# Kernel optimization log

Hardware: AMD Instinct MI355X
Metric: run time of the kernel (lower is better)

## Reference

```python
import jax, jax.numpy as jnp
import numpy as np


def setup_inputs() -> dict:
    key = jax.random.key(0)
    kq, kk, kv = jax.random.split(key, 3)
    shape = (4, 16, 2048, 64)  # [B, H, S, D]
    q = jax.random.normal(kq, shape, dtype=jnp.float32)
    k = jax.random.normal(kk, shape, dtype=jnp.float32)
    v = jax.random.normal(kv, shape, dtype=jnp.float32)
    return {"q": q, "k": k, "v": v}


def reference(q, k, v):
    d = q.shape[-1]
    scale = 1.0 / jnp.sqrt(jnp.asarray(d, dtype=q.dtype))
    # scores: [B, H, S, S]
    scores = jnp.einsum("bhqd,bhkd->bhqk", q, k) * scale
    probs = jax.nn.softmax(scores, axis=-1)
    # out: [B, H, S, D]
    return jnp.einsum("bhqk,bhkd->bhqd", probs, v)
```

## Files before the change

### kernel.cpp

```cpp
#include <hip/hip_runtime.h>
#include <hip/hip_bf16.h>
#include <stdint.h>

#define SEQ 2048
#define DH 64
#define QB 64
#define KB 64
#define NT (SEQ / KB)
#define PAD 72

typedef __attribute__((ext_vector_type(8))) short bf16x8;
typedef __attribute__((ext_vector_type(4))) short bf16x4;
typedef __attribute__((ext_vector_type(4))) float f32x4;

__device__ __forceinline__ short f2bf(float x) {
    union { __hip_bfloat16 h; short s; } u; u.h = __float2bfloat16(x); return u.s;
}
__device__ __forceinline__ int packbf(float lo, float hi) {
    return (int)((unsigned)(unsigned short)f2bf(lo) | ((unsigned)(unsigned short)f2bf(hi) << 16));
}

typedef __attribute__((address_space(3))) unsigned int       lds_u32;
typedef const __attribute__((address_space(1))) unsigned int g_u32;
__device__ __forceinline__ void gload16(const void* g, const void* lds_base) {
    __builtin_amdgcn_global_load_lds((g_u32*)(unsigned long long)g,
                                     (lds_u32*)(unsigned int)(unsigned long long)lds_base,
                                     16, 0, 0);
}

__global__ __launch_bounds__(256)
void prep_k_bf16(const float* __restrict__ K, short* __restrict__ Kb, int n8) {
    int i = blockIdx.x * 256 + threadIdx.x;
    if (i >= n8) return;
    float4 a = ((const float4*)K)[i * 2], b = ((const float4*)K)[i * 2 + 1];
    bf16x8 r;
    r[0]=f2bf(a.x); r[1]=f2bf(a.y); r[2]=f2bf(a.z); r[3]=f2bf(a.w);
    r[4]=f2bf(b.x); r[5]=f2bf(b.y); r[6]=f2bf(b.z); r[7]=f2bf(b.w);
    ((bf16x8*)Kb)[i] = r;
}

__global__ __launch_bounds__(256)
void prep_v_transpose(const float* __restrict__ V, short* __restrict__ VT) {
    __shared__ short tile[64][72];
    const int head = blockIdx.x >> 5;
    const int s0   = (blockIdx.x & 31) * 64;
    const int tid  = threadIdx.x;
    {
        const int r = tid >> 2, cb = (tid & 3) * 16;
        const float* src = V + ((size_t)head * SEQ + s0 + r) * DH + cb;
        float4 f0 = ((const float4*)src)[0], f1 = ((const float4*)src)[1];
        float4 f2 = ((const float4*)src)[2], f3 = ((const float4*)src)[3];
        bf16x8 lo, hi;
        lo[0]=f2bf(f0.x); lo[1]=f2bf(f0.y); lo[2]=f2bf(f0.z); lo[3]=f2bf(f0.w);
        lo[4]=f2bf(f1.x); lo[5]=f2bf(f1.y); lo[6]=f2bf(f1.z); lo[7]=f2bf(f1.w);
        hi[0]=f2bf(f2.x); hi[1]=f2bf(f2.y); hi[2]=f2bf(f2.z); hi[3]=f2bf(f2.w);
        hi[4]=f2bf(f3.x); hi[5]=f2bf(f3.y); hi[6]=f2bf(f3.z); hi[7]=f2bf(f3.w);
        *(bf16x8*)&tile[r][cb]     = lo;
        *(bf16x8*)&tile[r][cb + 8] = hi;
    }
    __syncthreads();
    {
        const int d = tid >> 2, sb = (tid & 3) * 16;
        bf16x8 lo, hi;
        #pragma unroll
        for (int j = 0; j < 8; ++j) lo[j] = tile[sb + j][d];
        #pragma unroll
        for (int j = 0; j < 8; ++j) hi[j] = tile[sb + 8 + j][d];
        short* dst = VT + ((size_t)head * DH + d) * SEQ + s0 + sb;
        *(bf16x8*)dst       = lo;
        *(bf16x8*)(dst + 8) = hi;
    }
}

__global__ __launch_bounds__(256)
void attn_fwd_v4(const float* __restrict__ Qp,
                 const short* __restrict__ Kb,
                 const short* __restrict__ VTb,
                 float* __restrict__ Op) {
    __shared__ __align__(16) short k_lds [2][KB * DH];
    __shared__ __align__(16) short vt_lds[2][DH * KB];

    const int tid  = threadIdx.x;
    const int wave = tid >> 6;
    const int lane = tid & 63;
    const int g    = lane >> 4;
    const int c    = lane & 15;

    const int chunk = gridDim.x >> 3;
    const int L     = (blockIdx.x & 7) * chunk + (blockIdx.x >> 3);
    const int head  = L >> 5;
    const int q0    = (L & 31) * QB + wave * 16;

    const size_t baseF  = (size_t)head * SEQ * DH;
    const short* Kh  = Kb  + baseF;
    const short* VTh = VTb + (size_t)head * DH * SEQ;

    const float qscale = 0.125f * 1.44269504088896f;
    bf16x8 qf[2];
    {
        const float* qrow = Qp + baseF + (size_t)(q0 + c) * DH;
        #pragma unroll
        for (int ch = 0; ch < 2; ++ch) {
            float4 a = *(const float4*)(qrow + ch * 32 + g * 8);
            float4 b = *(const float4*)(qrow + ch * 32 + g * 8 + 4);
            bf16x8 r;
            r[0]=f2bf(a.x*qscale); r[1]=f2bf(a.y*qscale); r[2]=f2bf(a.z*qscale); r[3]=f2bf(a.w*qscale);
            r[4]=f2bf(b.x*qscale); r[5]=f2bf(b.y*qscale); r[6]=f2bf(b.z*qscale); r[7]=f2bf(b.w*qscale);
            qf[ch] = r;
        }
    }

    f32x4 o_acc[4] = {};
    float m_run = -1e30f, l_run = 0.f;

    const int r8   = lane >> 3, c8 = lane & 7;
    const int csw8 = ((c8 ^ r8) << 3);
    const int rowb = 16 * wave;

    #define STAGE(T, BUF) do {                                                        \
        _Pragma("unroll")                                                             \
        for (int i = 0; i < 2; ++i) {                                                 \
            gload16(Kh  + ((size_t)((T) * KB + rowb + 8 * i + r8) * DH + csw8),       \
                    &k_lds[BUF][(rowb + 8 * i) * DH]);                                \
            gload16(VTh + ((size_t)(rowb + 8 * i + r8) * SEQ + (T) * KB + csw8),      \
                    &vt_lds[BUF][(rowb + 8 * i) * DH]);                               \
        } } while (0)

    STAGE(0, 0);
    __syncthreads();
    int cur = 0;

    for (int t = 0; t < NT; ++t) {
        if (t + 1 < NT) STAGE(t + 1, cur ^ 1);

        f32x4 sf[4];
        #pragma unroll
        for (int f = 0; f < 4; ++f) {
            f32x4 acc = {0.f, 0.f, 0.f, 0.f};
            #pragma unroll
            for (int ch = 0; ch < 2; ++ch) {
                bf16x8 kf = *(const bf16x8*)
                    &k_lds[cur][(16 * f + c) * DH + (((4 * ch + g) ^ (c & 7)) << 3)];
                acc = __builtin_amdgcn_mfma_f32_16x16x32_bf16(kf, qf[ch], acc, 0, 0, 0);
            }
            sf[f] = acc;
        }

        float mx = sf[0][0];
        #pragma unroll
        for (int f = 0; f < 4; ++f)
            #pragma unroll
            for (int r = 0; r < 4; ++r) mx = fmaxf(mx, sf[f][r]);
        mx = fmaxf(mx, __shfl_xor(mx, 16));
        mx = fmaxf(mx, __shfl_xor(mx, 32));
        const float mnew  = fmaxf(m_run, mx);
        const float alpha = exp2f(m_run - mnew);
        m_run = mnew;
        float rsum = 0.f;
        #pragma unroll
        for (int f = 0; f < 4; ++f)
            #pragma unroll
            for (int r = 0; r < 4; ++r) {
                float p = exp2f(sf[f][r] - mnew);
                sf[f][r] = p; rsum += p;
            }
        rsum += __shfl_xor(rsum, 16);
        rsum += __shfl_xor(rsum, 32);
        l_run = l_run * alpha + rsum;

        int pd[4][2];
        #pragma unroll
        for (int f = 0; f < 4; ++f) {
            pd[f][0] = packbf(sf[f][0], sf[f][1]);
            pd[f][1] = packbf(sf[f][2], sf[f][3]);
        }
        const int srcb = c + ((g & 1) << 5);
        const bool hi2 = (g >> 1) != 0;
        int a_dw[2][4];
        #pragma unroll
        for (int ch = 0; ch < 2; ++ch)
            #pragma unroll
            for (int jt = 0; jt < 4; ++jt) {
                int src = srcb + ((jt >> 1) << 4);
                int tA = __shfl(pd[2 * ch][jt & 1], src);
                int tB = __shfl(pd[2 * ch + 1][jt & 1], src);
                a_dw[ch][jt] = hi2 ? tB : tA;
            }

        float al[4];
        #pragma unroll
        for (int r = 0; r < 4; ++r) al[r] = __shfl(alpha, 4 * g + r);
        #pragma unroll
        for (int d16 = 0; d16 < 4; ++d16)
            #pragma unroll
            for (int r = 0; r < 4; ++r) o_acc[d16][r] *= al[r];

        #pragma unroll
        for (int ch = 0; ch < 2; ++ch) {
            union { int d[4]; bf16x8 v; } au;
            #pragma unroll
            for (int jt = 0; jt < 4; ++jt) au.d[jt] = a_dw[ch][jt];
            #pragma unroll
            for (int d16 = 0; d16 < 4; ++d16) {
                bf16x8 vf = *(const bf16x8*)
                    &vt_lds[cur][(16 * d16 + c) * DH + (((4 * ch + g) ^ (c & 7)) << 3)];
                o_acc[d16] = __builtin_amdgcn_mfma_f32_16x16x32_bf16(au.v, vf, o_acc[d16], 0, 0, 0);
            }
        }

        __syncthreads();
        cur ^= 1;
    }
    #undef STAGE

    #pragma unroll
    for (int r = 0; r < 4; ++r) {
        float li  = __shfl(l_run, 4 * g + r);
        float inv = 1.0f / li;
        float* orow = Op + baseF + (size_t)(q0 + 4 * g + r) * DH;
        #pragma unroll
        for (int d16 = 0; d16 < 4; ++d16)
            orow[d16 * 16 + c] = o_acc[d16][r] * inv;
    }
}

__global__ __launch_bounds__(256)
void attn_fwd_v3(const float* __restrict__ Qp, const float* __restrict__ Kp,
                 const float* __restrict__ Vp, float* __restrict__ Op) {
    __shared__ __align__(16) short k_lds[KB * PAD];
    __shared__ __align__(16) short vT_lds[DH * PAD];
    __shared__ __align__(16) short p_lds[4 * 16 * PAD];
    const int tid = threadIdx.x, wave = tid >> 6, lane = tid & 63;
    const int g = lane >> 4, c = lane & 15;
    const int chunk = gridDim.x >> 3;
    const int L = (blockIdx.x & 7) * chunk + (blockIdx.x >> 3);
    const int head = L >> 5;
    const int q0 = (L & 31) * QB + wave * 16;
    const size_t base = (size_t)head * SEQ * DH;
    const float qscale = 0.125f * 1.44269504088896f;
    bf16x8 qf[2];
    {
        const float* qrow = Qp + base + (size_t)(q0 + c) * DH;
        #pragma unroll
        for (int ch = 0; ch < 2; ++ch) {
            float4 a = *(const float4*)(qrow + ch * 32 + g * 8);
            float4 b = *(const float4*)(qrow + ch * 32 + g * 8 + 4);
            bf16x8 r;
            r[0]=f2bf(a.x*qscale); r[1]=f2bf(a.y*qscale); r[2]=f2bf(a.z*qscale); r[3]=f2bf(a.w*qscale);
            r[4]=f2bf(b.x*qscale); r[5]=f2bf(b.y*qscale); r[6]=f2bf(b.z*qscale); r[7]=f2bf(b.w*qscale);
            qf[ch] = r;
        }
    }
    f32x4 o_acc[4] = {};
    float m_run[4], l_run[4];
    #pragma unroll
    for (int r = 0; r < 4; ++r) { m_run[r] = -1e30f; l_run[r] = 0.f; }
    const int krow = tid >> 2, kcol = (tid & 3) << 4;
    const int vrow = (tid >> 4) << 2, vcol = (tid & 15) << 2;
    const float* kptr = Kp + base + (size_t)krow * DH + kcol;
    const float* vptr = Vp + base + (size_t)vrow * DH + vcol;
    float4 kr[4], vr[4];
    #pragma unroll
    for (int i = 0; i < 4; ++i) { kr[i] = ((const float4*)kptr)[i]; vr[i] = *(const float4*)(vptr + i * DH); }
    for (int t = 0; t < NT; ++t) {
        {
            bf16x8 lo, hi;
            lo[0]=f2bf(kr[0].x); lo[1]=f2bf(kr[0].y); lo[2]=f2bf(kr[0].z); lo[3]=f2bf(kr[0].w);
            lo[4]=f2bf(kr[1].x); lo[5]=f2bf(kr[1].y); lo[6]=f2bf(kr[1].z); lo[7]=f2bf(kr[1].w);
            hi[0]=f2bf(kr[2].x); hi[1]=f2bf(kr[2].y); hi[2]=f2bf(kr[2].z); hi[3]=f2bf(kr[2].w);
            hi[4]=f2bf(kr[3].x); hi[5]=f2bf(kr[3].y); hi[6]=f2bf(kr[3].z); hi[7]=f2bf(kr[3].w);
            *(bf16x8*)&k_lds[krow * PAD + kcol] = lo;
            *(bf16x8*)&k_lds[krow * PAD + kcol + 8] = hi;
            #pragma unroll
            for (int j = 0; j < 4; ++j) {
                bf16x4 w;
                w[0]=f2bf(((const float*)&vr[0])[j]); w[1]=f2bf(((const float*)&vr[1])[j]);
                w[2]=f2bf(((const float*)&vr[2])[j]); w[3]=f2bf(((const float*)&vr[3])[j]);
                *(bf16x4*)&vT_lds[(vcol + j) * PAD + vrow] = w;
            }
        }
        __syncthreads();
        if (t + 1 < NT) {
            const float* kn = kptr + (size_t)(t + 1) * KB * DH;
            const float* vn = vptr + (size_t)(t + 1) * KB * DH;
            #pragma unroll
            for (int i = 0; i < 4; ++i) { kr[i] = ((const float4*)kn)[i]; vr[i] = *(const float4*)(vn + i * DH); }
        }
        f32x4 sf[4];
        #pragma unroll
        for (int f = 0; f < 4; ++f) {
            f32x4 acc = {0.f, 0.f, 0.f, 0.f};
            #pragma unroll
            for (int ch = 0; ch < 2; ++ch) {
                bf16x8 kf = *(const bf16x8*)&k_lds[(f * 16 + c) * PAD + ch * 32 + g * 8];
                acc = __builtin_amdgcn_mfma_f32_16x16x32_bf16(qf[ch], kf, acc, 0, 0, 0);
            }
            sf[f] = acc;
        }
        short* pw = &p_lds[wave * 16 * PAD];
        #pragma unroll
        for (int r = 0; r < 4; ++r) {
            float mx = fmaxf(fmaxf(sf[0][r], sf[1][r]), fmaxf(sf[2][r], sf[3][r]));
            #pragma unroll
            for (int mk = 1; mk < 16; mk <<= 1) mx = fmaxf(mx, __shfl_xor(mx, mk));
            const float mnew = fmaxf(m_run[r], mx);
            const float alpha = exp2f(m_run[r] - mnew);
            m_run[r] = mnew;
            float rsum = 0.f;
            #pragma unroll
            for (int f = 0; f < 4; ++f) { float p = exp2f(sf[f][r] - mnew); sf[f][r] = p; rsum += p; }
            #pragma unroll
            for (int mk = 1; mk < 16; mk <<= 1) rsum += __shfl_xor(rsum, mk);
            l_run[r] = l_run[r] * alpha + rsum;
            #pragma unroll
            for (int d16 = 0; d16 < 4; ++d16) o_acc[d16][r] *= alpha;
            #pragma unroll
            for (int f = 0; f < 4; ++f) pw[(4 * g + r) * PAD + f * 16 + c] = f2bf(sf[f][r]);
        }
        asm volatile("" ::: "memory");
        #pragma unroll
        for (int ch = 0; ch < 2; ++ch) {
            bf16x8 pf = *(const bf16x8*)&pw[c * PAD + ch * 32 + g * 8];
            #pragma unroll
            for (int d16 = 0; d16 < 4; ++d16) {
                bf16x8 vf = *(const bf16x8*)&vT_lds[(d16 * 16 + c) * PAD + ch * 32 + g * 8];
                o_acc[d16] = __builtin_amdgcn_mfma_f32_16x16x32_bf16(pf, vf, o_acc[d16], 0, 0, 0);
            }
        }
        __syncthreads();
    }
    #pragma unroll
    for (int r = 0; r < 4; ++r) {
        const float inv = 1.0f / l_run[r];
        float* orow = Op + base + (size_t)(q0 + 4 * g + r) * DH;
        #pragma unroll
        for (int d16 = 0; d16 < 4; ++d16) orow[d16 * 16 + c] = o_acc[d16][r] * inv;
    }
}

extern "C" void kernel_launch(void* const* d_in, const int* in_sizes, int n_in,
                              void* d_out, int out_size, void* d_ws, size_t ws_size,
                              hipStream_t stream) {
    const float* q = (const float*)d_in[0];
    const float* k = (const float*)d_in[1];
    const float* v = (const float*)d_in[2];
    float* out = (float*)d_out;
    const int bh = in_sizes[0] / (SEQ * DH);
    const size_t nelem = (size_t)bh * SEQ * DH;
    const size_t need  = nelem * 2 * 2;

    if (ws_size >= need) {
        short* Kb  = (short*)d_ws;
        short* VTb = Kb + nelem;
        int n8 = (int)(nelem / 8);
        prep_k_bf16   <<<(n8 + 255) / 256, 256, 0, stream>>>(k, Kb, n8);
        prep_v_transpose<<<bh * (SEQ / 64), 256, 0, stream>>>(v, VTb);
        attn_fwd_v4   <<<(SEQ / QB) * bh, 256, 0, stream>>>(q, Kb, VTb, out);
    } else {
        attn_fwd_v3   <<<(SEQ / QB) * bh, 256, 0, stream>>>(q, k, v, out);
    }
}
```

Before: 296.2 us.

## Fuse prep kernels, add lazy softmax rescale, unroll tile loop, set MFMA priority

Merges the K conversion and V transpose kernels into a single launch, saving one launch and its tail. In the attention kernel, the online softmax skips rescaling the output accumulator unless some row's max grows by more than 8 in log2 units, which removes most per-tile multiplies and one exp. It also unrolls the tile loop by two so LDS buffer indices are compile-time constants, precomputes the swizzled LDS offsets, and raises wave priority around the MFMA blocks. The lazy rescale lets exponentials reach up to 2^8 before renormalising, a known FA-style trick that is safe for fp32 accumulators.

```diff
diff --git a/kernel.cpp b/kernel.cpp
--- a/kernel.cpp
+++ b/kernel.cpp
@@ -29,21 +29,23 @@
 }
 
 __global__ __launch_bounds__(256)
-void prep_k_bf16(const float* __restrict__ K, short* __restrict__ Kb, int n8) {
-    int i = blockIdx.x * 256 + threadIdx.x;
-    if (i >= n8) return;
-    float4 a = ((const float4*)K)[i * 2], b = ((const float4*)K)[i * 2 + 1];
-    bf16x8 r;
-    r[0]=f2bf(a.x); r[1]=f2bf(a.y); r[2]=f2bf(a.z); r[3]=f2bf(a.w);
-    r[4]=f2bf(b.x); r[5]=f2bf(b.y); r[6]=f2bf(b.z); r[7]=f2bf(b.w);
-    ((bf16x8*)Kb)[i] = r;
-}
-
-__global__ __launch_bounds__(256)
-void prep_v_transpose(const float* __restrict__ V, short* __restrict__ VT) {
+void prep_fused(const float* __restrict__ K, const float* __restrict__ V,
+                short* __restrict__ Kb, short* __restrict__ VT,
+                int nKblocks, int n8) {
+    if ((int)blockIdx.x < nKblocks) {
+        int i = blockIdx.x * 256 + threadIdx.x;
+        if (i >= n8) return;
+        float4 a = ((const float4*)K)[i * 2], b = ((const float4*)K)[i * 2 + 1];
+        bf16x8 r;
+        r[0]=f2bf(a.x); r[1]=f2bf(a.y); r[2]=f2bf(a.z); r[3]=f2bf(a.w);
+        r[4]=f2bf(b.x); r[5]=f2bf(b.y); r[6]=f2bf(b.z); r[7]=f2bf(b.w);
+        ((bf16x8*)Kb)[i] = r;
+        return;
+    }
     __shared__ short tile[64][72];
-    const int head = blockIdx.x >> 5;
-    const int s0   = (blockIdx.x & 31) * 64;
+    const int vb   = blockIdx.x - nKblocks;
+    const int head = vb >> 5;
+    const int s0   = (vb & 31) * 64;
     const int tid  = threadIdx.x;
     {
         const int r = tid >> 2, cb = (tid & 3) * 16;
@@ -73,7 +75,7 @@
 }
 
 __global__ __launch_bounds__(256)
-void attn_fwd_v4(const float* __restrict__ Qp,
+void attn_fwd_v5(const float* __restrict__ Qp,
                  const short* __restrict__ Kb,
                  const short* __restrict__ VTb,
                  float* __restrict__ Op) {
@@ -113,6 +115,12 @@
     f32x4 o_acc[4] = {};
     float m_run = -1e30f, l_run = 0.f;
 
+    const int kbase0 = c * DH + (((0 + g) ^ (c & 7)) << 3);
+    const int kbase1 = c * DH + (((4 + g) ^ (c & 7)) << 3);
+
+    const int srcb = c + ((g & 1) << 5);
+    const bool hi2 = (g >> 1) != 0;
+
     const int r8   = lane >> 3, c8 = lane & 7;
     const int csw8 = ((c8 ^ r8) << 3);
     const int rowb = 16 * wave;
@@ -126,91 +134,94 @@
                     &vt_lds[BUF][(rowb + 8 * i) * DH]);                               \
         } } while (0)
 
+    #define TILE_BODY(T, BUF) do {                                                   \
+        if ((T) + 1 < NT) STAGE((T) + 1, (BUF) ^ 1);                                  \
+        f32x4 sf[4];                                                                  \
+        __builtin_amdgcn_s_setprio(1);                                                \
+        _Pragma("unroll")                                                             \
+        for (int f = 0; f < 4; ++f) {                                                 \
+            f32x4 acc = {0.f, 0.f, 0.f, 0.f};                                         \
+            {   bf16x8 kf = *(const bf16x8*)&k_lds[BUF][f * 1024 + kbase0];           \
+                acc = __builtin_amdgcn_mfma_f32_16x16x32_bf16(kf, qf[0], acc, 0,0,0); \
+                kf = *(const bf16x8*)&k_lds[BUF][f * 1024 + kbase1];                  \
+                acc = __builtin_amdgcn_mfma_f32_16x16x32_bf16(kf, qf[1], acc, 0,0,0); \
+            }                                                                         \
+            sf[f] = acc;                                                              \
+        }                                                                             \
+        __builtin_amdgcn_s_setprio(0);                                                \
+        float mx = sf[0][0];                                                          \
+        _Pragma("unroll")                                                             \
+        for (int f = 0; f < 4; ++f)                                                   \
+            _Pragma("unroll")                                                         \
+            for (int r = 0; r < 4; ++r) mx = fmaxf(mx, sf[f][r]);                     \
+        mx = fmaxf(mx, __shfl_xor(mx, 16));                                           \
+        mx = fmaxf(mx, __shfl_xor(mx, 32));                                           \
+        if (!__all(mx - m_run <= 8.0f)) {                          \
+            const float mnew  = fmaxf(m_run, mx);                                     \
+            const float alpha = exp2f(m_run - mnew);                                  \
+            float al[4];                                                              \
+            _Pragma("unroll")                                                         \
+            for (int r = 0; r < 4; ++r) al[r] = __shfl(alpha, 4 * g + r);             \
+            _Pragma("unroll")                                                         \
+            for (int d16 = 0; d16 < 4; ++d16)                                         \
+                _Pragma("unroll")                                                     \
+                for (int r = 0; r < 4; ++r) o_acc[d16][r] *= al[r];                   \
+            l_run *= alpha;                                                           \
+            m_run = mnew;                                                             \
+        }                                                                             \
+        float rsum = 0.f;                                                             \
+        _Pragma("unroll")                                                             \
+        for (int f = 0; f < 4; ++f)                                                   \
+            _Pragma("unroll")                                                         \
+            for (int r = 0; r < 4; ++r) {                                             \
+                float p = exp2f(sf[f][r] - m_run);                                    \
+                sf[f][r] = p; rsum += p;                                              \
+            }                                                                         \
+        rsum += __shfl_xor(rsum, 16);                                                 \
+        rsum += __shfl_xor(rsum, 32);                                                 \
+        l_run += rsum;                                                                \
+        int pd[4][2];                                                                 \
+        _Pragma("unroll")                                                             \
+        for (int f = 0; f < 4; ++f) {                                                 \
+            pd[f][0] = packbf(sf[f][0], sf[f][1]);                                    \
+            pd[f][1] = packbf(sf[f][2], sf[f][3]);                                    \
+        }                                                                             \
+        int a_dw[2][4];                                                               \
+        _Pragma("unroll")                                                             \
+        for (int ch = 0; ch < 2; ++ch)                                                \
+            _Pragma("unroll")                                                         \
+            for (int jt = 0; jt < 4; ++jt) {                                          \
+                int src = srcb + ((jt >> 1) << 4);                                    \
+                int tA = __shfl(pd[2 * ch][jt & 1], src);                             \
+                int tB = __shfl(pd[2 * ch + 1][jt & 1], src);                         \
+                a_dw[ch][jt] = hi2 ? tB : tA;                                         \
+            }                                                                         \
+        __builtin_amdgcn_s_setprio(1);                                                \
+        _Pragma("unroll")                                                             \
+        for (int ch = 0; ch < 2; ++ch) {                                              \
+            union { int d[4]; bf16x8 v; } au;                                         \
+            _Pragma("unroll")                                                         \
+            for (int jt = 0; jt < 4; ++jt) au.d[jt] = a_dw[ch][jt];                   \
+            _Pragma("unroll")                                                         \
+            for (int d16 = 0; d16 < 4; ++d16) {                                       \
+                bf16x8 vf = *(const bf16x8*)&vt_lds[BUF][d16 * 1024 +                 \
+                                                         (ch ? kbase1 : kbase0)];     \
+                o_acc[d16] = __builtin_amdgcn_mfma_f32_16x16x32_bf16(au.v, vf,        \
+                                                                o_acc[d16], 0,0,0);   \
+            }                                                                         \
+        }                                                                             \
+        __builtin_amdgcn_s_setprio(0);                                                \
+        __syncthreads();                                                              \
+    } while (0)
+
     STAGE(0, 0);
     __syncthreads();
-    int cur = 0;
-
-    for (int t = 0; t < NT; ++t) {
-        if (t + 1 < NT) STAGE(t + 1, cur ^ 1);
-
-        f32x4 sf[4];
-        #pragma unroll
-        for (int f = 0; f < 4; ++f) {
-            f32x4 acc = {0.f, 0.f, 0.f, 0.f};
-            #pragma unroll
-            for (int ch = 0; ch < 2; ++ch) {
-                bf16x8 kf = *(const bf16x8*)
-                    &k_lds[cur][(16 * f + c) * DH + (((4 * ch + g) ^ (c & 7)) << 3)];
-                acc = __builtin_amdgcn_mfma_f32_16x16x32_bf16(kf, qf[ch], acc, 0, 0, 0);
-            }
-            sf[f] = acc;
-        }
-
-        float mx = sf[0][0];
-        #pragma unroll
-        for (int f = 0; f < 4; ++f)
-            #pragma unroll
-            for (int r = 0; r < 4; ++r) mx = fmaxf(mx, sf[f][r]);
-        mx = fmaxf(mx, __shfl_xor(mx, 16));
-        mx = fmaxf(mx, __shfl_xor(mx, 32));
-        const float mnew  = fmaxf(m_run, mx);
-        const float alpha = exp2f(m_run - mnew);
-        m_run = mnew;
-        float rsum = 0.f;
-        #pragma unroll
-        for (int f = 0; f < 4; ++f)
-            #pragma unroll
-            for (int r = 0; r < 4; ++r) {
-                float p = exp2f(sf[f][r] - mnew);
-                sf[f][r] = p; rsum += p;
-            }
-        rsum += __shfl_xor(rsum, 16);
-        rsum += __shfl_xor(rsum, 32);
-        l_run = l_run * alpha + rsum;
-
-        int pd[4][2];
-        #pragma unroll
-        for (int f = 0; f < 4; ++f) {
-            pd[f][0] = packbf(sf[f][0], sf[f][1]);
-            pd[f][1] = packbf(sf[f][2], sf[f][3]);
-        }
-        const int srcb = c + ((g & 1) << 5);
-        const bool hi2 = (g >> 1) != 0;
-        int a_dw[2][4];
-        #pragma unroll
-        for (int ch = 0; ch < 2; ++ch)
-            #pragma unroll
-            for (int jt = 0; jt < 4; ++jt) {
-                int src = srcb + ((jt >> 1) << 4);
-                int tA = __shfl(pd[2 * ch][jt & 1], src);
-                int tB = __shfl(pd[2 * ch + 1][jt & 1], src);
-                a_dw[ch][jt] = hi2 ? tB : tA;
-            }
-
-        float al[4];
-        #pragma unroll
-        for (int r = 0; r < 4; ++r) al[r] = __shfl(alpha, 4 * g + r);
-        #pragma unroll
-        for (int d16 = 0; d16 < 4; ++d16)
-            #pragma unroll
-            for (int r = 0; r < 4; ++r) o_acc[d16][r] *= al[r];
-
-        #pragma unroll
-        for (int ch = 0; ch < 2; ++ch) {
-            union { int d[4]; bf16x8 v; } au;
-            #pragma unroll
-            for (int jt = 0; jt < 4; ++jt) au.d[jt] = a_dw[ch][jt];
-            #pragma unroll
-            for (int d16 = 0; d16 < 4; ++d16) {
-                bf16x8 vf = *(const bf16x8*)
-                    &vt_lds[cur][(16 * d16 + c) * DH + (((4 * ch + g) ^ (c & 7)) << 3)];
-                o_acc[d16] = __builtin_amdgcn_mfma_f32_16x16x32_bf16(au.v, vf, o_acc[d16], 0, 0, 0);
-            }
-        }
-
-        __syncthreads();
-        cur ^= 1;
-    }
+
+    for (int t = 0; t < NT; t += 2) {
+        TILE_BODY(t, 0);
+        TILE_BODY(t + 1, 1);
+    }
+    #undef TILE_BODY
     #undef STAGE
 
     #pragma unroll
@@ -352,11 +363,12 @@
     if (ws_size >= need) {
         short* Kb  = (short*)d_ws;
         short* VTb = Kb + nelem;
-        int n8 = (int)(nelem / 8);
-        prep_k_bf16   <<<(n8 + 255) / 256, 256, 0, stream>>>(k, Kb, n8);
-        prep_v_transpose<<<bh * (SEQ / 64), 256, 0, stream>>>(v, VTb);
-        attn_fwd_v4   <<<(SEQ / QB) * bh, 256, 0, stream>>>(q, Kb, VTb, out);
+        const int n8       = (int)(nelem / 8);
+        const int nKblocks = (n8 + 255) / 256;
+        const int nVblocks = bh * (SEQ / 64);
+        prep_fused <<<nKblocks + nVblocks, 256, 0, stream>>>(k, v, Kb, VTb, nKblocks, n8);
+        attn_fwd_v5<<<(SEQ / QB) * bh, 256, 0, stream>>>(q, Kb, VTb, out);
     } else {
-        attn_fwd_v3   <<<(SEQ / QB) * bh, 256, 0, stream>>>(q, k, v, out);
-    }
-}
+        attn_fwd_v3<<<(SEQ / QB) * bh, 256, 0, stream>>>(q, k, v, out);
+    }
+}
```

Result: faster. 285.8 us (-3.5%).
